# Optimization experiments

Measured on AMD Instinct MI355X. Metric: run time of the kernel, lower is better.

## Reference

```python
import jax, jax.numpy as jnp
import numpy as np

B, S, D = 16, 2048, 128

def setup_inputs() -> dict:
    key = jax.random.key(0)
    k1, k2, k3, k4 = jax.random.split(key, 4)
    q = jax.random.normal(k1, (B, S, D), dtype=jnp.float32)
    k = jax.random.normal(k2, (B, S, D), dtype=jnp.float32)
    v = jax.random.normal(k3, (B, S, D), dtype=jnp.float32)
    scale = jnp.float32(1.0 / np.sqrt(D))
    attn_mask = jax.random.randint(k4, (B, S, S), 0, 2).astype(jnp.bool_)
    return {"q": q, "k": k, "v": v, "scale": scale, "attn_mask": attn_mask}

def reference(q, k, v, scale, attn_mask):
    # attention scores: [B, Sq, Sk]
    scores = jnp.einsum('bqd,bkd->bqk', q, k) * scale
    # masked_fill(attn_mask, -inf): True positions are masked out
    scores = jnp.where(attn_mask, -jnp.inf, scores)
    attention = jax.nn.softmax(scores, axis=2)
    # dropout prob = 0.0 -> identity
    context = jnp.einsum('bqk,bkd->bqd', attention, v)
    return (context, attention)
```

## Files before the change

### kernel.cpp

```cpp
#include <hip/hip_runtime.h>
#include <hip/hip_bf16.h>
#include <hip/hip_fp16.h>

#define B_ 16
#define S_ 2048
#define D_ 128
#define QB 64
#define KT 64
#define NT_ 32
#define LOG2E 1.4426950408889634f

typedef __attribute__((ext_vector_type(8))) short short8;
typedef __attribute__((ext_vector_type(8))) unsigned short u16x8;
typedef __attribute__((ext_vector_type(4))) float f32x4;
typedef __attribute__((ext_vector_type(4))) float f32x4v;
typedef __attribute__((ext_vector_type(4))) int i32x4;
typedef __attribute__((ext_vector_type(4))) unsigned short u16x4;

__device__ __forceinline__ float exp2fast(float x) {
  return __builtin_amdgcn_exp2f(x);
}
__device__ __forceinline__ unsigned short f2bf(float f) {
  unsigned int u = __builtin_bit_cast(unsigned int, f);
  unsigned int r = (u + 0x7fffu + ((u >> 16) & 1u)) >> 16;
  return (unsigned short)r;
}
__device__ __forceinline__ float bf2f(unsigned short h) {
  return __builtin_bit_cast(float, (unsigned int)h << 16);
}
__device__ __forceinline__ int swz_bid(int bid, int nwg) {
  int cpx = nwg >> 3;
  return (bid & 7) * cpx + (bid >> 3);
}

__global__ void cvt_bf16_kernel(const float* __restrict__ x,
                                unsigned short* __restrict__ y,
                                const float* __restrict__ sc, float postmul,
                                int n4) {
  int i = blockIdx.x * blockDim.x + threadIdx.x;
  if (i >= n4) return;
  float s = (sc ? sc[0] : 1.0f) * postmul;
  float4 f = reinterpret_cast<const float4*>(x)[i];
  u16x4 o;
  o[0] = f2bf(f.x * s); o[1] = f2bf(f.y * s);
  o[2] = f2bf(f.z * s); o[3] = f2bf(f.w * s);
  reinterpret_cast<u16x4*>(y)[i] = o;
}

__global__ void vtrans_kernel(const float* __restrict__ v,
                              unsigned short* __restrict__ vT) {
  __shared__ float tile[32][33];
  int b = blockIdx.z, kt = blockIdx.x, dt = blockIdx.y;
  int t = threadIdx.x;
  int c = t & 31, r0 = t >> 5;
  const float* src = v + ((size_t)b * S_ + (size_t)kt * 32) * D_ + dt * 32;
#pragma unroll
  for (int i = 0; i < 4; i++) {
    int r = r0 + 8 * i;
    tile[r][c] = src[(size_t)r * D_ + c];
  }
  __syncthreads();
  unsigned short* dst = vT + ((size_t)b * D_ + dt * 32) * S_ + (size_t)kt * 32;
#pragma unroll
  for (int i = 0; i < 4; i++) {
    int r = r0 + 8 * i;
    dst[(size_t)r * S_ + c] = f2bf(tile[c][r]);
  }
}

__global__ __launch_bounds__(512, 4)
void attn_main_kernel(const unsigned short* __restrict__ qbf,
                      const unsigned short* __restrict__ kbf,
                      const unsigned short* __restrict__ vTb,
                      const void* __restrict__ maskp,
                      float* __restrict__ ctx,
                      float* __restrict__ att) {
  __shared__ __align__(16) char kbuf[2][KT * 256];
  __shared__ __align__(16) char vbuf[2][D_ * 128];
  __shared__ __align__(16) char etile[QB * 128];
  __shared__ float zpart[8][2][16];
  __shared__ float iz_l[QB];

  const int tid = threadIdx.x;
  const int bid = swz_bid(blockIdx.x, B_ * (S_ / QB));
  const int b  = bid >> 5;
  const int q0 = (bid & 31) << 6;

  const int w   = tid >> 6;
  const int l   = tid & 63;
  const int l16 = l & 15;
  const int lq  = l >> 4;
  const int qh  = w & 1;
  const int kq  = w >> 1;

  int myv = 0;
  if (tid < 256) myv = (reinterpret_cast<const unsigned int*>(maskp)[tid] > 1u) ? 1 : 0;
  const int mask_is_byte = __syncthreads_or(myv);

  short8 qf[2][4];
#pragma unroll
  for (int qg = 0; qg < 2; ++qg) {
    const unsigned short* qp =
        qbf + (((size_t)(b * S_ + q0 + qh * 32 + qg * 16 + l16)) << 7) + lq * 8;
#pragma unroll
    for (int ks = 0; ks < 4; ks++)
      qf[qg][ks] = *reinterpret_cast<const short8*>(qp + ks * 32);
  }

  const unsigned char* mask8 = reinterpret_cast<const unsigned char*>(maskp);
  const int* mask32 = reinterpret_cast<const int*>(maskp);
  size_t mrowq[2];
#pragma unroll
  for (int qg = 0; qg < 2; ++qg)
    mrowq[qg] = ((size_t)b * S_ + q0 + qh * 32 + qg * 16 + l16) * S_ + kq * 16 + lq * 4;

  const char* kbb = reinterpret_cast<const char*>(kbf + (((size_t)b * S_) << 7));
  const char* vbb = reinterpret_cast<const char*>(vTb + ((size_t)b * D_) * S_);

  const int krow_s = tid >> 3, kcol_s = (tid & 7) * 32;
  const int vrow_s = tid >> 2, vcol_s = (tid & 3) * 32;
  const size_t ksrc_off = (size_t)krow_s * 256 + kcol_s;
  const size_t vsrc_off = (size_t)vrow_s * (S_ * 2) + vcol_s;
  const int kswz = (krow_s & 15) << 4, vswz = (vrow_s & 7) << 4;

  u16x8 stk0, stk1, stv0, stv1;
  stk0 = *reinterpret_cast<const u16x8*>(kbb + ksrc_off);
  stk1 = *reinterpret_cast<const u16x8*>(kbb + ksrc_off + 16);
  {
    char* kd = &kbuf[0][0] + krow_s * 256;
    *reinterpret_cast<u16x8*>(kd + (kcol_s ^ kswz)) = stk0;
    *reinterpret_cast<u16x8*>(kd + ((kcol_s + 16) ^ kswz)) = stk1;
  }
  __syncthreads();

  unsigned int mbits[8] = {0, 0, 0, 0, 0, 0, 0, 0};
  float Zl[2] = {0.0f, 0.0f};
  const int krow_f = kq * 16 + l16;
  const int kfx = (krow_f & 15) << 4;

  for (int t = 0; t < NT_; ++t) {
    const int cur = t & 1;
    if (t < NT_ - 1) {
      const char* src = kbb + ((size_t)(t + 1) * KT * 256);
      stk0 = *reinterpret_cast<const u16x8*>(src + ksrc_off);
      stk1 = *reinterpret_cast<const u16x8*>(src + ksrc_off + 16);
    }
    unsigned int nib[2];
    if (mask_is_byte) {
#pragma unroll
      for (int qg = 0; qg < 2; ++qg) {
        unsigned int mv = *reinterpret_cast<const unsigned int*>(
            mask8 + mrowq[qg] + t * KT);
        nib[qg] = ((mv & 0x000000ffu) ? 1u : 0u) | ((mv & 0x0000ff00u) ? 2u : 0u) |
                  ((mv & 0x00ff0000u) ? 4u : 0u) | ((mv & 0xff000000u) ? 8u : 0u);
      }
    } else {
#pragma unroll
      for (int qg = 0; qg < 2; ++qg) {
        i32x4 mi = *reinterpret_cast<const i32x4*>(mask32 + mrowq[qg] + t * KT);
        nib[qg] = (mi[0] ? 1u : 0u) | (mi[1] ? 2u : 0u) |
                  (mi[2] ? 4u : 0u) | (mi[3] ? 8u : 0u);
      }
    }
    mbits[t >> 2] |= (nib[0] | (nib[1] << 4)) << ((t & 3) * 8);

    const char* kp = &kbuf[cur][0] + krow_f * 256;
    f32x4 a0 = {0.f, 0.f, 0.f, 0.f}, a1 = {0.f, 0.f, 0.f, 0.f};
    __builtin_amdgcn_s_setprio(1);
#pragma unroll
    for (int ks = 0; ks < 4; ++ks) {
      short8 kfr = *reinterpret_cast<const short8*>(kp + ((ks * 64 + lq * 16) ^ kfx));
      a0 = __builtin_amdgcn_mfma_f32_16x16x32_bf16(kfr, qf[0][ks], a0, 0, 0, 0);
      a1 = __builtin_amdgcn_mfma_f32_16x16x32_bf16(kfr, qf[1][ks], a1, 0, 0, 0);
    }
    __builtin_amdgcn_s_setprio(0);
#pragma unroll
    for (int r = 0; r < 4; ++r) {
      if (!((nib[0] >> r) & 1u)) Zl[0] += exp2fast(a0[r]);
      if (!((nib[1] >> r) & 1u)) Zl[1] += exp2fast(a1[r]);
    }
    if (t < NT_ - 1) {
      char* kd = &kbuf[cur ^ 1][0] + krow_s * 256;
      *reinterpret_cast<u16x8*>(kd + (kcol_s ^ kswz)) = stk0;
      *reinterpret_cast<u16x8*>(kd + ((kcol_s + 16) ^ kswz)) = stk1;
    }
    __syncthreads();
  }

  stk0 = *reinterpret_cast<const u16x8*>(kbb + ksrc_off);
  stk1 = *reinterpret_cast<const u16x8*>(kbb + ksrc_off + 16);
  stv0 = *reinterpret_cast<const u16x8*>(vbb + vsrc_off);
  stv1 = *reinterpret_cast<const u16x8*>(vbb + vsrc_off + 16);
#pragma unroll
  for (int qg = 0; qg < 2; ++qg) {
    Zl[qg] += __shfl_xor(Zl[qg], 16, 64);
    Zl[qg] += __shfl_xor(Zl[qg], 32, 64);
  }
  if (lq == 0) { zpart[w][0][l16] = Zl[0]; zpart[w][1][l16] = Zl[1]; }
  __syncthreads();
  if (tid < QB) {
    const int qh_ = tid >> 5, qg_ = (tid >> 4) & 1, r_ = tid & 15;
    float Z = 0.0f;
#pragma unroll
    for (int kk = 0; kk < 4; ++kk) Z += zpart[kk * 2 + qh_][qg_][r_];
    iz_l[tid] = 1.0f / Z;
  }
  {
    char* kd = &kbuf[0][0] + krow_s * 256;
    *reinterpret_cast<u16x8*>(kd + (kcol_s ^ kswz)) = stk0;
    *reinterpret_cast<u16x8*>(kd + ((kcol_s + 16) ^ kswz)) = stk1;
    char* vd = &vbuf[0][0] + vrow_s * 128;
    *reinterpret_cast<u16x8*>(vd + (vcol_s ^ vswz)) = stv0;
    *reinterpret_cast<u16x8*>(vd + ((vcol_s + 16) ^ vswz)) = stv1;
  }
  __syncthreads();

  const float izq0 = iz_l[qh * 32 + l16];
  const float izq1 = iz_l[qh * 32 + 16 + l16];

  f32x4 apv[2][2] = {{{0.f,0.f,0.f,0.f},{0.f,0.f,0.f,0.f}},
                     {{0.f,0.f,0.f,0.f},{0.f,0.f,0.f,0.f}}};
  for (int t = 0; t < NT_; ++t) {
    const int cur = t & 1;
    if (t < NT_ - 1) {
      const char* src = kbb + ((size_t)(t + 1) * KT * 256);
      stk0 = *reinterpret_cast<const u16x8*>(src + ksrc_off);
      stk1 = *reinterpret_cast<const u16x8*>(src + ksrc_off + 16);
      const char* vs2 = vbb + (size_t)(t + 1) * 128;
      stv0 = *reinterpret_cast<const u16x8*>(vs2 + vsrc_off);
      stv1 = *reinterpret_cast<const u16x8*>(vs2 + vsrc_off + 16);
    }
    const char* kp = &kbuf[cur][0] + krow_f * 256;
    f32x4 a0 = {0.f, 0.f, 0.f, 0.f}, a1 = {0.f, 0.f, 0.f, 0.f};
    __builtin_amdgcn_s_setprio(1);
#pragma unroll
    for (int ks = 0; ks < 4; ++ks) {
      short8 kfr = *reinterpret_cast<const short8*>(kp + ((ks * 64 + lq * 16) ^ kfx));
      a0 = __builtin_amdgcn_mfma_f32_16x16x32_bf16(kfr, qf[0][ks], a0, 0, 0, 0);
      a1 = __builtin_amdgcn_mfma_f32_16x16x32_bf16(kfr, qf[1][ks], a1, 0, 0, 0);
    }
    __builtin_amdgcn_s_setprio(0);
    const unsigned int nibs = mbits[t >> 2] >> ((t & 3) * 8);
    u16x4 eb[2];
#pragma unroll
    for (int r = 0; r < 4; ++r) {
      eb[0][r] = f2bf((nibs & (1u << r)) ? 0.0f : exp2fast(a0[r]) * izq0);
      eb[1][r] = f2bf((nibs & (16u << r)) ? 0.0f : exp2fast(a1[r]) * izq1);
    }
    __syncthreads();
#pragma unroll
    for (int qg = 0; qg < 2; ++qg) {
      const int re = qh * 32 + qg * 16 + l16;
      *reinterpret_cast<u16x4*>(
          etile + re * 128 + ((kq * 32 + lq * 8) ^ ((re & 7) << 4))) = eb[qg];
    }
    if (t < NT_ - 1) {
      char* kd = &kbuf[cur ^ 1][0] + krow_s * 256;
      *reinterpret_cast<u16x8*>(kd + (kcol_s ^ kswz)) = stk0;
      *reinterpret_cast<u16x8*>(kd + ((kcol_s + 16) ^ kswz)) = stk1;
      char* vd = &vbuf[cur ^ 1][0] + vrow_s * 128;
      *reinterpret_cast<u16x8*>(vd + (vcol_s ^ vswz)) = stv0;
      *reinterpret_cast<u16x8*>(vd + ((vcol_s + 16) ^ vswz)) = stv1;
    }
    __syncthreads();
#pragma unroll
    for (int h = 0; h < 2; ++h) {
      const int re = w * 8 + h * 4 + (l >> 4);
      u16x4 ev = *reinterpret_cast<const u16x4*>(
          etile + re * 128 + (((l & 15) * 8) ^ ((re & 7) << 4)));
      f32x4v pv;
#pragma unroll
      for (int j = 0; j < 4; ++j) pv[j] = bf2f(ev[j]);
      __builtin_nontemporal_store(pv, reinterpret_cast<f32x4v*>(
          att + ((size_t)(b * S_ + q0 + re)) * S_ + t * KT + (l & 15) * 4));
    }
#pragma unroll
    for (int kk = 0; kk < 2; ++kk) {
      short8 afr[2], bfr[2];
#pragma unroll
      for (int qg = 0; qg < 2; ++qg) {
        const int re = qh * 32 + qg * 16 + l16;
        afr[qg] = *reinterpret_cast<const short8*>(
            etile + re * 128 + ((kk * 64 + lq * 16) ^ ((re & 7) << 4)));
      }
#pragma unroll
      for (int dg = 0; dg < 2; ++dg) {
        const int vr = kq * 32 + dg * 16 + l16;
        bfr[dg] = *reinterpret_cast<const short8*>(
            &vbuf[cur][0] + vr * 128 + ((kk * 64 + lq * 16) ^ ((vr & 7) << 4)));
      }
      __builtin_amdgcn_s_setprio(1);
#pragma unroll
      for (int qg = 0; qg < 2; ++qg)
#pragma unroll
        for (int dg = 0; dg < 2; ++dg)
          apv[qg][dg] = __builtin_amdgcn_mfma_f32_16x16x32_bf16(
              afr[qg], bfr[dg], apv[qg][dg], 0, 0, 0);
      __builtin_amdgcn_s_setprio(0);
    }
  }

#pragma unroll
  for (int qg = 0; qg < 2; ++qg) {
#pragma unroll
    for (int dg = 0; dg < 2; ++dg) {
#pragma unroll
      for (int r = 0; r < 4; ++r) {
        __builtin_nontemporal_store(
            apv[qg][dg][r],
            ctx + ((size_t)(b * S_ + q0 + qh * 32 + qg * 16 + lq * 4 + r)) * D_ +
                kq * 32 + dg * 16 + l16);
      }
    }
  }
}

extern "C" void kernel_launch(void* const* d_in, const int* in_sizes, int n_in,
                              void* d_out, int out_size, void* d_ws, size_t ws_size,
                              hipStream_t stream) {
  (void)in_sizes; (void)n_in; (void)out_size; (void)ws_size;
  const float* q = (const float*)d_in[0];
  const float* k = (const float*)d_in[1];
  const float* v = (const float*)d_in[2];
  const float* scale = (const float*)d_in[3];
  const void* mask = d_in[4];

  const size_t qkv_elems = (size_t)B_ * S_ * D_;
  unsigned short* qbf = (unsigned short*)d_ws;
  unsigned short* kbf = qbf + qkv_elems;
  unsigned short* vTb = kbf + qkv_elems;

  float* ctx = (float*)d_out;
  float* att = ctx + (size_t)B_ * S_ * D_;

  const int n4 = B_ * S_ * D_ / 4;
  cvt_bf16_kernel<<<dim3((n4 + 255) / 256), dim3(256), 0, stream>>>(
      q, qbf, scale, LOG2E, n4);
  cvt_bf16_kernel<<<dim3((n4 + 255) / 256), dim3(256), 0, stream>>>(
      k, kbf, nullptr, 1.0f, n4);
  vtrans_kernel<<<dim3(S_ / 32, D_ / 32, B_), dim3(256), 0, stream>>>(v, vTb);
  attn_main_kernel<<<dim3(B_ * (S_ / QB)), dim3(512), 0, stream>>>(
      qbf, kbf, vTb, mask, ctx, att);
}
```

Before: 162.8 us.

## Load K and V tiles directly into LDS with global_load_lds

```diff
diff --git a/kernel.cpp b/kernel.cpp
--- a/kernel.cpp
+++ b/kernel.cpp
@@ -11,7 +11,6 @@
 #define LOG2E 1.4426950408889634f
 
 typedef __attribute__((ext_vector_type(8))) short short8;
-typedef __attribute__((ext_vector_type(8))) unsigned short u16x8;
 typedef __attribute__((ext_vector_type(4))) float f32x4;
 typedef __attribute__((ext_vector_type(4))) float f32x4v;
 typedef __attribute__((ext_vector_type(4))) int i32x4;
@@ -27,6 +26,11 @@
 }
 __device__ __forceinline__ float bf2f(unsigned short h) {
   return __builtin_bit_cast(float, (unsigned int)h << 16);
+}
+__device__ __forceinline__ void gl16(const void* g, void* l) {
+  __builtin_amdgcn_global_load_lds(
+      (const __attribute__((address_space(1))) unsigned int*)g,
+      (__attribute__((address_space(3))) unsigned int*)l, 16, 0, 0);
 }
 __device__ __forceinline__ int swz_bid(int bid, int nwg) {
   int cpx = nwg >> 3;
@@ -93,6 +97,18 @@
   const int qh  = w & 1;
   const int kq  = w >> 1;
 
+  const char* kbb = reinterpret_cast<const char*>(kbf + (((size_t)b * S_) << 7));
+  const char* vbb = reinterpret_cast<const char*>(vTb + ((size_t)b * D_) * S_);
+
+  const int krow_g = w * 4 + (l >> 4);
+  const size_t ksrc = (size_t)krow_g * 256 + (((l & 15) * 16) ^ ((krow_g & 15) << 4));
+  const int vrow_g = w * 8 + (l >> 3);
+  const size_t vsrc = (size_t)vrow_g * (S_ * 2) + (((l & 7) * 16) ^ ((vrow_g & 7) << 4));
+  const int ldsoff = w * 1024;
+
+  gl16(kbb + ksrc,        &kbuf[0][0] + ldsoff);
+  gl16(kbb + ksrc + 8192, &kbuf[0][0] + ldsoff + 8192);
+
   int myv = 0;
   if (tid < 256) myv = (reinterpret_cast<const unsigned int*>(maskp)[tid] > 1u) ? 1 : 0;
   const int mask_is_byte = __syncthreads_or(myv);
@@ -113,25 +129,6 @@
 #pragma unroll
   for (int qg = 0; qg < 2; ++qg)
     mrowq[qg] = ((size_t)b * S_ + q0 + qh * 32 + qg * 16 + l16) * S_ + kq * 16 + lq * 4;
-
-  const char* kbb = reinterpret_cast<const char*>(kbf + (((size_t)b * S_) << 7));
-  const char* vbb = reinterpret_cast<const char*>(vTb + ((size_t)b * D_) * S_);
-
-  const int krow_s = tid >> 3, kcol_s = (tid & 7) * 32;
-  const int vrow_s = tid >> 2, vcol_s = (tid & 3) * 32;
-  const size_t ksrc_off = (size_t)krow_s * 256 + kcol_s;
-  const size_t vsrc_off = (size_t)vrow_s * (S_ * 2) + vcol_s;
-  const int kswz = (krow_s & 15) << 4, vswz = (vrow_s & 7) << 4;
-
-  u16x8 stk0, stk1, stv0, stv1;
-  stk0 = *reinterpret_cast<const u16x8*>(kbb + ksrc_off);
-  stk1 = *reinterpret_cast<const u16x8*>(kbb + ksrc_off + 16);
-  {
-    char* kd = &kbuf[0][0] + krow_s * 256;
-    *reinterpret_cast<u16x8*>(kd + (kcol_s ^ kswz)) = stk0;
-    *reinterpret_cast<u16x8*>(kd + ((kcol_s + 16) ^ kswz)) = stk1;
-  }
-  __syncthreads();
 
   unsigned int mbits[8] = {0, 0, 0, 0, 0, 0, 0, 0};
   float Zl[2] = {0.0f, 0.0f};
@@ -141,9 +138,9 @@
   for (int t = 0; t < NT_; ++t) {
     const int cur = t & 1;
     if (t < NT_ - 1) {
-      const char* src = kbb + ((size_t)(t + 1) * KT * 256);
-      stk0 = *reinterpret_cast<const u16x8*>(src + ksrc_off);
-      stk1 = *reinterpret_cast<const u16x8*>(src + ksrc_off + 16);
+      const char* src = kbb + (size_t)(t + 1) * (KT * 256);
+      gl16(src + ksrc,        &kbuf[cur ^ 1][0] + ldsoff);
+      gl16(src + ksrc + 8192, &kbuf[cur ^ 1][0] + ldsoff + 8192);
     }
     unsigned int nib[2];
     if (mask_is_byte) {
@@ -179,18 +176,13 @@
       if (!((nib[0] >> r) & 1u)) Zl[0] += exp2fast(a0[r]);
       if (!((nib[1] >> r) & 1u)) Zl[1] += exp2fast(a1[r]);
     }
-    if (t < NT_ - 1) {
-      char* kd = &kbuf[cur ^ 1][0] + krow_s * 256;
-      *reinterpret_cast<u16x8*>(kd + (kcol_s ^ kswz)) = stk0;
-      *reinterpret_cast<u16x8*>(kd + ((kcol_s + 16) ^ kswz)) = stk1;
-    }
     __syncthreads();
   }
 
-  stk0 = *reinterpret_cast<const u16x8*>(kbb + ksrc_off);
-  stk1 = *reinterpret_cast<const u16x8*>(kbb + ksrc_off + 16);
-  stv0 = *reinterpret_cast<const u16x8*>(vbb + vsrc_off);
-  stv1 = *reinterpret_cast<const u16x8*>(vbb + vsrc_off + 16);
+  gl16(kbb + ksrc,          &kbuf[0][0] + ldsoff);
+  gl16(kbb + ksrc + 8192,   &kbuf[0][0] + ldsoff + 8192);
+  gl16(vbb + vsrc,          &vbuf[0][0] + ldsoff);
+  gl16(vbb + vsrc + 262144, &vbuf[0][0] + ldsoff + 8192);
 #pragma unroll
   for (int qg = 0; qg < 2; ++qg) {
     Zl[qg] += __shfl_xor(Zl[qg], 16, 64);
@@ -205,14 +197,6 @@
     for (int kk = 0; kk < 4; ++kk) Z += zpart[kk * 2 + qh_][qg_][r_];
     iz_l[tid] = 1.0f / Z;
   }
-  {
-    char* kd = &kbuf[0][0] + krow_s * 256;
-    *reinterpret_cast<u16x8*>(kd + (kcol_s ^ kswz)) = stk0;
-    *reinterpret_cast<u16x8*>(kd + ((kcol_s + 16) ^ kswz)) = stk1;
-    char* vd = &vbuf[0][0] + vrow_s * 128;
-    *reinterpret_cast<u16x8*>(vd + (vcol_s ^ vswz)) = stv0;
-    *reinterpret_cast<u16x8*>(vd + ((vcol_s + 16) ^ vswz)) = stv1;
-  }
   __syncthreads();
 
   const float izq0 = iz_l[qh * 32 + l16];
@@ -223,12 +207,9 @@
   for (int t = 0; t < NT_; ++t) {
     const int cur = t & 1;
     if (t < NT_ - 1) {
-      const char* src = kbb + ((size_t)(t + 1) * KT * 256);
-      stk0 = *reinterpret_cast<const u16x8*>(src + ksrc_off);
-      stk1 = *reinterpret_cast<const u16x8*>(src + ksrc_off + 16);
-      const char* vs2 = vbb + (size_t)(t + 1) * 128;
-      stv0 = *reinterpret_cast<const u16x8*>(vs2 + vsrc_off);
-      stv1 = *reinterpret_cast<const u16x8*>(vs2 + vsrc_off + 16);
+      const char* src = kbb + (size_t)(t + 1) * (KT * 256);
+      gl16(src + ksrc,        &kbuf[cur ^ 1][0] + ldsoff);
+      gl16(src + ksrc + 8192, &kbuf[cur ^ 1][0] + ldsoff + 8192);
     }
     const char* kp = &kbuf[cur][0] + krow_f * 256;
     f32x4 a0 = {0.f, 0.f, 0.f, 0.f}, a1 = {0.f, 0.f, 0.f, 0.f};
@@ -253,14 +234,6 @@
       const int re = qh * 32 + qg * 16 + l16;
       *reinterpret_cast<u16x4*>(
           etile + re * 128 + ((kq * 32 + lq * 8) ^ ((re & 7) << 4))) = eb[qg];
-    }
-    if (t < NT_ - 1) {
-      char* kd = &kbuf[cur ^ 1][0] + krow_s * 256;
-      *reinterpret_cast<u16x8*>(kd + (kcol_s ^ kswz)) = stk0;
-      *reinterpret_cast<u16x8*>(kd + ((kcol_s + 16) ^ kswz)) = stk1;
-      char* vd = &vbuf[cur ^ 1][0] + vrow_s * 128;
-      *reinterpret_cast<u16x8*>(vd + (vcol_s ^ vswz)) = stv0;
-      *reinterpret_cast<u16x8*>(vd + ((vcol_s + 16) ^ vswz)) = stv1;
     }
     __syncthreads();
 #pragma unroll
@@ -297,6 +270,11 @@
           apv[qg][dg] = __builtin_amdgcn_mfma_f32_16x16x32_bf16(
               afr[qg], bfr[dg], apv[qg][dg], 0, 0, 0);
       __builtin_amdgcn_s_setprio(0);
+    }
+    if (t < NT_ - 1) {
+      const char* vs2 = vbb + (size_t)(t + 1) * 128;
+      gl16(vs2 + vsrc,          &vbuf[cur ^ 1][0] + ldsoff);
+      gl16(vs2 + vsrc + 262144, &vbuf[cur ^ 1][0] + ldsoff + 8192);
     }
   }
 
```

New measurement: 159.9 us. No clear change (-1.8%).
